# Kernel optimization log

Hardware: AMD Instinct MI355X
Metric: run time of the kernel (lower is better)

Reference implementation:

```python
import jax, jax.numpy as jnp
import numpy as np

N_NODES = 10000
N_EDGES = 640000
NODE_DIM = 128
EDGE_DIM = 64


def setup_inputs() -> dict:
    key = jax.random.key(0)
    k1, k2, k3, k4, k5 = jax.random.split(key, 5)
    atom_embedding = jax.random.normal(k1, (N_NODES, NODE_DIM), dtype=jnp.float32)
    edge_embedding = jax.random.normal(k2, (N_EDGES, EDGE_DIM), dtype=jnp.float32)
    src_idx = jax.random.randint(k3, (N_EDGES,), 0, N_NODES, dtype=jnp.int64)
    # Linear(node_dim+edge_dim -> node_dim); store weight as [in, out]
    W = jax.random.normal(k4, (NODE_DIM + EDGE_DIM, NODE_DIM), dtype=jnp.float32) / np.sqrt(NODE_DIM + EDGE_DIM)
    b = jax.random.normal(k5, (NODE_DIM,), dtype=jnp.float32) * 0.01
    return {"atom_embedding": atom_embedding, "edge_embedding": edge_embedding,
            "src_idx": src_idx, "W": W, "b": b}


def reference(atom_embedding, edge_embedding, src_idx, W, b):
    # Gather source-node features per edge: [n_edges, node_dim]
    src_feat = atom_embedding[src_idx]
    # Concat with edge features: [n_edges, node_dim + edge_dim]
    h = jnp.concatenate([src_feat, edge_embedding], axis=-1)
    # DenseLayer: Linear + ReLU -> [n_edges, node_dim]
    return jax.nn.relu(h @ W + b)
```

## Files before the change

kernel.cpp:

```cpp
#include <hip/hip_runtime.h>

#define N_EDGES   640000
#define NODE_DIM  128
#define EDGE_DIM  64
#define K_DIM     192
#define LDS_K     196

typedef float  f32x16 __attribute__((ext_vector_type(16)));
typedef __bf16 bf16x8 __attribute__((ext_vector_type(8)));

union FragU {
  uint   u[4];
  bf16x8 b;
};

__device__ __forceinline__ ushort f2bf_rne(float f) {
  uint u = __builtin_bit_cast(uint, f);
  return (ushort)((u + 0x7fffu + ((u >> 16) & 1u)) >> 16);
}

__device__ __forceinline__ uint pack2bf(float f0, float f1) {
  uint u0 = __builtin_bit_cast(uint, f0) + 0x8000u;
  uint u1 = __builtin_bit_cast(uint, f1) + 0x8000u;
  return __builtin_amdgcn_perm(u1, u0, 0x07060302u);
}

__global__ __launch_bounds__(256, 2) void a2b_kernel(
    const float* __restrict__ atom, const float* __restrict__ edgef,
    const int* __restrict__ srcidx, const float* __restrict__ W,
    const float* __restrict__ bias, float* __restrict__ out) {
  __shared__ ushort WT[NODE_DIM * LDS_K];

  for (int i = threadIdx.x; i < K_DIM * NODE_DIM; i += 256) {
    int k = i >> 7, n = i & 127;
    WT[n * LDS_K + k] = f2bf_rne(W[i]);
  }
  __syncthreads();

  const int wave = threadIdx.x >> 6;
  const int lane = threadIdx.x & 63;
  const int eloc = lane & 31;
  const int half = lane >> 5;
  const int ebase = (blockIdx.x * 4 + wave) * 32;
  const int e = ebase + eloc;
  const int s = srcidx[e];
  const float* arow = atom  + (size_t)s * NODE_DIM;
  const float* erow = edgef + (size_t)e * EDGE_DIM;

  float4 fA[12][2];
#pragma unroll
  for (int ks = 0; ks < 12; ks++) {
    const int k0 = ks * 16 + half * 8;
    const float* p = (ks < 8) ? (arow + k0) : (erow + (k0 - 128));
    fA[ks][0] = *(const float4*)p;
    fA[ks][1] = *(const float4*)(p + 4);
  }

  f32x16 acc[4];
#pragma unroll
  for (int nt = 0; nt < 4; nt++)
#pragma unroll
    for (int i = 0; i < 16; i++) acc[nt][i] = 0.f;

#pragma unroll
  for (int ks = 0; ks < 12; ks++) {
    FragU a;
    a.u[0] = pack2bf(fA[ks][0].x, fA[ks][0].y);
    a.u[1] = pack2bf(fA[ks][0].z, fA[ks][0].w);
    a.u[2] = pack2bf(fA[ks][1].x, fA[ks][1].y);
    a.u[3] = pack2bf(fA[ks][1].z, fA[ks][1].w);
    const int kof = ks * 16 + half * 8;
#pragma unroll
    for (int nt = 0; nt < 4; nt++) {
      const uint2* bp = (const uint2*)&WT[(nt * 32 + eloc) * LDS_K + kof];
      uint2 b0 = bp[0], b1 = bp[1];
      FragU bf_;
      bf_.u[0] = b0.x; bf_.u[1] = b0.y; bf_.u[2] = b1.x; bf_.u[3] = b1.y;
      acc[nt] = __builtin_amdgcn_mfma_f32_32x32x16_bf16(a.b, bf_.b, acc[nt], 0, 0, 0);
    }
  }

#pragma unroll
  for (int nt = 0; nt < 4; nt++) {
    const int col = nt * 32 + eloc;
    const float bb = bias[col];
#pragma unroll
    for (int r = 0; r < 16; r++) {
      const int row = (r & 3) + 8 * (r >> 2) + 4 * half;
      const float v = acc[nt][r] + bb;
      out[(size_t)(ebase + row) * NODE_DIM + col] = fmaxf(v, 0.f);
    }
  }
}

extern "C" void kernel_launch(void* const* d_in, const int* in_sizes, int n_in,
                              void* d_out, int out_size, void* d_ws, size_t ws_size,
                              hipStream_t stream) {
  const float* atom   = (const float*)d_in[0];
  const float* edgef  = (const float*)d_in[1];
  const int*   srcidx = (const int*)d_in[2];
  const float* W      = (const float*)d_in[3];
  const float* bias   = (const float*)d_in[4];
  float* out = (float*)d_out;

  dim3 grid(N_EDGES / 128);
  dim3 block(256);
  hipLaunchKernelGGL(a2b_kernel, grid, block, 0, stream,
                     atom, edgef, srcidx, W, bias, out);
}
```

Baseline: 495.9 us.

## Precompute bf16 weight transpose once and make main kernel persistent over edge tiles

A separate prep kernel converts and transposes W to bf16 in workspace once per call. The main kernel is now a persistent grid of 1000 blocks, each looping over 5 edge tiles. Each block copies the prepared weights into LDS with vector loads, so the per-block W conversion is paid 1000 times instead of 5000. It also prefetches the next source index and raises occupancy to 3 blocks per CU. The risks are fewer waves in flight to hide the gather latency, plus the cost of an extra kernel launch.

```diff
diff --git a/kernel.cpp b/kernel.cpp
--- a/kernel.cpp
+++ b/kernel.cpp
@@ -5,6 +5,9 @@
 #define EDGE_DIM  64
 #define K_DIM     192
 #define LDS_K     196
+#define GRID      1000
+#define WPB       4
+#define ITERS     (N_EDGES / 32 / (GRID * WPB))
 
 typedef float  f32x16 __attribute__((ext_vector_type(16)));
 typedef __bf16 bf16x8 __attribute__((ext_vector_type(8)));
@@ -25,15 +28,27 @@
   return __builtin_amdgcn_perm(u1, u0, 0x07060302u);
 }
 
-__global__ __launch_bounds__(256, 2) void a2b_kernel(
+__global__ __launch_bounds__(256) void prep_w(const float* __restrict__ W,
+                                              ushort* __restrict__ WTg) {
+  int i = blockIdx.x * 256 + threadIdx.x;
+  if (i >= K_DIM * NODE_DIM) return;
+  int k = i >> 7, n = i & 127;
+  WTg[n * LDS_K + k] = f2bf_rne(W[i]);
+}
+
+__global__ __launch_bounds__(256, 3) void a2b_main(
     const float* __restrict__ atom, const float* __restrict__ edgef,
-    const int* __restrict__ srcidx, const float* __restrict__ W,
+    const int* __restrict__ srcidx, const ushort* __restrict__ WTg,
     const float* __restrict__ bias, float* __restrict__ out) {
   __shared__ ushort WT[NODE_DIM * LDS_K];
 
-  for (int i = threadIdx.x; i < K_DIM * NODE_DIM; i += 256) {
-    int k = i >> 7, n = i & 127;
-    WT[n * LDS_K + k] = f2bf_rne(W[i]);
+  {
+    const uint4* s4 = (const uint4*)WTg;
+    uint4* d4 = (uint4*)WT;
+#pragma unroll
+    for (int i = 0; i < 12; i++) d4[threadIdx.x + i * 256] = s4[threadIdx.x + i * 256];
+    int r = 3072 + threadIdx.x;
+    if (r < 3136) d4[r] = s4[r];
   }
   __syncthreads();
 
@@ -41,55 +56,80 @@
   const int lane = threadIdx.x & 63;
   const int eloc = lane & 31;
   const int half = lane >> 5;
-  const int ebase = (blockIdx.x * 4 + wave) * 32;
-  const int e = ebase + eloc;
-  const int s = srcidx[e];
-  const float* arow = atom  + (size_t)s * NODE_DIM;
-  const float* erow = edgef + (size_t)e * EDGE_DIM;
 
-  float4 fA[12][2];
+  float bb[4];
 #pragma unroll
-  for (int ks = 0; ks < 12; ks++) {
-    const int k0 = ks * 16 + half * 8;
-    const float* p = (ks < 8) ? (arow + k0) : (erow + (k0 - 128));
-    fA[ks][0] = *(const float4*)p;
-    fA[ks][1] = *(const float4*)(p + 4);
-  }
+  for (int nt = 0; nt < 4; nt++) bb[nt] = bias[nt * 32 + eloc];
 
-  f32x16 acc[4];
+  const int gw = blockIdx.x * WPB + wave;
+  int e = gw * 32 + eloc;
+  int s = srcidx[e];
+
+  for (int it = 0; it < ITERS; ++it) {
+    const int ebase = e - eloc;
+    const float* arow = atom  + (size_t)s * NODE_DIM;
+    const float* erow = edgef + (size_t)e * EDGE_DIM;
+
+    uint aF[12][4];
 #pragma unroll
-  for (int nt = 0; nt < 4; nt++)
+    for (int ph = 0; ph < 4; ++ph) {
+      float4 v[3][2];
 #pragma unroll
-    for (int i = 0; i < 16; i++) acc[nt][i] = 0.f;
+      for (int j = 0; j < 3; ++j) {
+        const int ks = ph * 3 + j;
+        const int k0 = ks * 16 + half * 8;
+        const float* p = (ks < 8) ? (arow + k0) : (erow + (k0 - 128));
+        v[j][0] = *(const float4*)p;
+        v[j][1] = *(const float4*)(p + 4);
+      }
+#pragma unroll
+      for (int j = 0; j < 3; ++j) {
+        const int ks = ph * 3 + j;
+        aF[ks][0] = pack2bf(v[j][0].x, v[j][0].y);
+        aF[ks][1] = pack2bf(v[j][0].z, v[j][0].w);
+        aF[ks][2] = pack2bf(v[j][1].x, v[j][1].y);
+        aF[ks][3] = pack2bf(v[j][1].z, v[j][1].w);
+      }
+    }
+
+    const int e_next = e + GRID * WPB * 32;
+    int s_next = 0;
+    if (it + 1 < ITERS) s_next = srcidx[e_next];
+
+    f32x16 acc[4];
+#pragma unroll
+    for (int nt = 0; nt < 4; nt++)
+#pragma unroll
+      for (int i = 0; i < 16; i++) acc[nt][i] = 0.f;
 
 #pragma unroll
-  for (int ks = 0; ks < 12; ks++) {
-    FragU a;
-    a.u[0] = pack2bf(fA[ks][0].x, fA[ks][0].y);
-    a.u[1] = pack2bf(fA[ks][0].z, fA[ks][0].w);
-    a.u[2] = pack2bf(fA[ks][1].x, fA[ks][1].y);
-    a.u[3] = pack2bf(fA[ks][1].z, fA[ks][1].w);
-    const int kof = ks * 16 + half * 8;
+    for (int ks = 0; ks < 12; ks++) {
+      FragU a;
+      a.u[0] = aF[ks][0]; a.u[1] = aF[ks][1];
+      a.u[2] = aF[ks][2]; a.u[3] = aF[ks][3];
+      const int kof = ks * 16 + half * 8;
+#pragma unroll
+      for (int nt = 0; nt < 4; nt++) {
+        const uint2* bp = (const uint2*)&WT[(nt * 32 + eloc) * LDS_K + kof];
+        uint2 b0 = bp[0], b1 = bp[1];
+        FragU bf_;
+        bf_.u[0] = b0.x; bf_.u[1] = b0.y; bf_.u[2] = b1.x; bf_.u[3] = b1.y;
+        acc[nt] = __builtin_amdgcn_mfma_f32_32x32x16_bf16(a.b, bf_.b, acc[nt], 0, 0, 0);
+      }
+    }
+
 #pragma unroll
     for (int nt = 0; nt < 4; nt++) {
-      const uint2* bp = (const uint2*)&WT[(nt * 32 + eloc) * LDS_K + kof];
-      uint2 b0 = bp[0], b1 = bp[1];
-      FragU bf_;
-      bf_.u[0] = b0.x; bf_.u[1] = b0.y; bf_.u[2] = b1.x; bf_.u[3] = b1.y;
-      acc[nt] = __builtin_amdgcn_mfma_f32_32x32x16_bf16(a.b, bf_.b, acc[nt], 0, 0, 0);
+      const int col = nt * 32 + eloc;
+#pragma unroll
+      for (int r = 0; r < 16; r++) {
+        const int row = (r & 3) + 8 * (r >> 2) + 4 * half;
+        out[(size_t)(ebase + row) * NODE_DIM + col] = fmaxf(acc[nt][r] + bb[nt], 0.f);
+      }
     }
-  }
 
-#pragma unroll
-  for (int nt = 0; nt < 4; nt++) {
-    const int col = nt * 32 + eloc;
-    const float bb = bias[col];
-#pragma unroll
-    for (int r = 0; r < 16; r++) {
-      const int row = (r & 3) + 8 * (r >> 2) + 4 * half;
-      const float v = acc[nt][r] + bb;
-      out[(size_t)(ebase + row) * NODE_DIM + col] = fmaxf(v, 0.f);
-    }
+    e = e_next;
+    s = s_next;
   }
 }
 
@@ -101,10 +141,10 @@
   const int*   srcidx = (const int*)d_in[2];
   const float* W      = (const float*)d_in[3];
   const float* bias   = (const float*)d_in[4];
-  float* out = (float*)d_out;
+  float* out   = (float*)d_out;
+  ushort* WTg  = (ushort*)d_ws;
 
-  dim3 grid(N_EDGES / 128);
-  dim3 block(256);
-  hipLaunchKernelGGL(a2b_kernel, grid, block, 0, stream,
-                     atom, edgef, srcidx, W, bias, out);
+  hipLaunchKernelGGL(prep_w, dim3(96), dim3(256), 0, stream, W, WTg);
+  hipLaunchKernelGGL(a2b_main, dim3(GRID), dim3(256), 0, stream,
+                     atom, edgef, srcidx, WTg, bias, out);
 }
```

New measurement: 628.7 us. +26.8%, slower.
